# Performance work log

Hardware: AMD Instinct MI355X
Metric: run time of the kernel (lower is better)

The kernel has to match this reference:

```python
import jax, jax.numpy as jnp
import numpy as np

N = 100000
E = 1600000
F_IN = 256   # 4 * 64 after concat
H = 128

def _glorot(key, shape):
    fan_in, fan_out = shape
    lim = jnp.sqrt(6.0 / (fan_in + fan_out))
    return jax.random.uniform(key, shape, jnp.float32, -lim, lim)

def setup_inputs() -> dict:
    key = jax.random.key(0)
    ks = jax.random.split(key, 32)
    inp = {
        'x': jax.random.normal(ks[0], (N, 64), jnp.float32),
        'diff': jax.random.normal(ks[1], (N, 64), jnp.float32),
        'rec_prev': jax.random.normal(ks[2], (N, 64), jnp.float32),
        'hidden_prev': jax.random.normal(ks[3], (N, 64), jnp.float32),
        'edge_index': jax.random.randint(ks[4], (2, E), 0, N, jnp.int64),
    }
    dims = [(F_IN, H), (H, H), (H, H), (H, 1)]
    for i, (din, dout) in enumerate(dims):
        inp[f'Wl{i}'] = _glorot(ks[5 + 3 * i], (din, dout))  # neighbor (aggr) weight
        inp[f'Wr{i}'] = _glorot(ks[6 + 3 * i], (din, dout))  # root weight
        inp[f'b{i}'] = jnp.zeros((dout,), jnp.float32)
    return inp

def _sage_conv(h, src, dst, Wl, Wr, b):
    # mean aggregation of source-node features at destination nodes (PyG SAGEConv)
    msg_sum = jax.ops.segment_sum(h[src], dst, num_segments=N)        # [N, F]
    cnt = jax.ops.segment_sum(jnp.ones((src.shape[0],), h.dtype), dst, num_segments=N)
    mean = msg_sum / jnp.maximum(cnt, 1.0)[:, None]
    return mean @ Wl + h @ Wr + b

def reference(x, diff, rec_prev, hidden_prev, edge_index,
              Wl0, Wr0, b0, Wl1, Wr1, b1, Wl2, Wr2, b2, Wl3, Wr3, b3):
    src, dst = edge_index[0], edge_index[1]
    h = jnp.concatenate([x, diff, rec_prev, hidden_prev], axis=1)  # [N, 256]
    params = [(Wl0, Wr0, b0), (Wl1, Wr1, b1), (Wl2, Wr2, b2), (Wl3, Wr3, b3)]
    h = _sage_conv(h, src, dst, *params[0])
    for Wl, Wr, b in params[1:]:
        h = jax.nn.relu(h)
        h = _sage_conv(h, src, dst, Wl, Wr, b)
    out = jax.nn.sigmoid(h)          # [N, 1]
    lwp_util = jnp.mean(out)
    return out, lwp_util
```

## Files before the change

kernel.cpp:

```cpp
#include <hip/hip_runtime.h>
#include <hip/hip_bf16.h>

#define NN 100000
#define EE 1600000
#define HH 128
#define NB 391
#define CAP 5120
#define GB 1563
#define SB 256
#define EPB (EE / SB)

typedef short bf16x8 __attribute__((ext_vector_type(8)));
typedef short bf16x4 __attribute__((ext_vector_type(4)));
typedef float f32x4  __attribute__((ext_vector_type(4)));

__device__ inline short f2bf(float v) {
    __hip_bfloat16 b = __float2bfloat16(v);
    return *reinterpret_cast<short*>(&b);
}

typedef __attribute__((address_space(1))) void gvoid_t;
typedef __attribute__((address_space(3))) void svoid_t;
__device__ __forceinline__ void gload16(const void* g, void* l) {
    __builtin_amdgcn_global_load_lds((gvoid_t*)g, (svoid_t*)l, 16, 0, 0);
}

__device__ __forceinline__ void ld_fence() { asm volatile("" ::: "memory"); }

template <int N>
__device__ __forceinline__ void wait_vm_bar() {
    if constexpr (N == 0)
        asm volatile("s_waitcnt vmcnt(0)\n\ts_barrier" ::: "memory");
    else if constexpr (N == 2)
        asm volatile("s_waitcnt vmcnt(2)\n\ts_barrier" ::: "memory");
    else if constexpr (N == 4)
        asm volatile("s_waitcnt vmcnt(4)\n\ts_barrier" ::: "memory");
    else if constexpr (N == 8)
        asm volatile("s_waitcnt vmcnt(8)\n\ts_barrier" ::: "memory");
    else if constexpr (N == 12)
        asm volatile("s_waitcnt vmcnt(12)\n\ts_barrier" ::: "memory");
    else
        static_assert(N == 0 || N == 2 || N == 4 || N == 8 || N == 12, "bad N");
}
__device__ __forceinline__ void barrier_only() {
    asm volatile("s_barrier" ::: "memory");
}

__global__ __launch_bounds__(1024) void prep_kernel(
    const float* __restrict__ Wl0, const float* __restrict__ Wr0,
    const float* __restrict__ Wl1, const float* __restrict__ Wr1,
    const float* __restrict__ Wl2, const float* __restrict__ Wr2,
    __hip_bfloat16* __restrict__ WT0, __hip_bfloat16* __restrict__ WT1,
    __hip_bfloat16* __restrict__ WT2, int* __restrict__ bcur) {
    const int t = threadIdx.x;
    if (blockIdx.x == 128) {
        if (t < NB) bcur[t] = 0;
        return;
    }
    int id = blockIdx.x * 1024 + t;
    if (id < 65536) {
        int k = id & 255, n = id >> 8;
        float v = (n < 128) ? Wl0[(size_t)k * 128 + n]
                            : Wr0[(size_t)k * 128 + (n - 128)];
        WT0[(size_t)n * 256 + k] = __float2bfloat16(v);
    } else {
        id -= 65536;
        int layer = id >> 15;
        int u = id & 32767;
        int k = u & 127, n = u >> 7;
        const float* Wl = layer ? Wl2 : Wl1;
        const float* Wr = layer ? Wr2 : Wr1;
        __hip_bfloat16* WT = layer ? WT2 : WT1;
        float v = (n < 128) ? Wl[(size_t)k * 128 + n]
                            : Wr[(size_t)k * 128 + (n - 128)];
        WT[(size_t)n * 128 + k] = __float2bfloat16(v);
    }
}

#define EW 264
template <int K, bool FIRST>
__device__ __forceinline__ void gemm_body(
    short* __restrict__ lsh, int bid,
    const __hip_bfloat16* hin,
    const float* __restrict__ x0, const float* __restrict__ x1,
    const float* __restrict__ x2, const float* __restrict__ x3,
    const __hip_bfloat16* __restrict__ wt, const float* __restrict__ bias,
    __hip_bfloat16* zout, __hip_bfloat16* __restrict__ rout) {
    const int t    = threadIdx.x;
    const int w    = t >> 6;
    const int lane = t & 63;
    const int quad = lane >> 4;
    const int l16  = lane & 15;
    const int n0   = bid * 64;

    constexpr int NS   = K / 64;
    constexpr int BUFB = FIRST ? 16384 : 8192;
    char* const lc = (char*)lsh;

    const __hip_bfloat16* afeat[4];
#pragma unroll
    for (int ft = 0; ft < 4; ++ft)
        afeat[ft] = wt + (size_t)(w * 64 + ft * 16 + l16) * K + quad * 8;

    f32x4 acc[4][4];
#pragma unroll
    for (int ft = 0; ft < 4; ++ft)
#pragma unroll
        for (int nt = 0; nt < 4; ++nt)
            acc[ft][nt] = (f32x4){0.f, 0.f, 0.f, 0.f};

    bf16x8 wreg[NS][8];

    auto loadW = [&](int p) {
#pragma unroll
        for (int kcl = 0; kcl < 2; ++kcl)
#pragma unroll
            for (int ft = 0; ft < 4; ++ft)
                wreg[p][kcl * 4 + ft] =
                    *(const bf16x8*)(afeat[ft] + (p * 2 + kcl) * 32);
    };

    auto stage = [&](int p) {
        char* lb = lc + p * BUFB;
        if constexpr (FIRST) {
            const float* sp = (p == 0) ? x0 : (p == 1) ? x1 : (p == 2) ? x2 : x3;
#pragma unroll
            for (int i = 0; i < 4; ++i) {
                const int j   = w * 4 + i;
                const int row = j * 4 + (lane >> 4);
                int rg = n0 + row; if (rg > NN - 1) rg = NN - 1;
                const int colb = ((lane & 15) * 16) ^ ((row & 15) << 4);
                gload16((const char*)sp + (size_t)rg * 256 + colb, lb + j * 1024);
            }
        } else {
#pragma unroll
            for (int i = 0; i < 2; ++i) {
                const int j   = w * 2 + i;
                const int row = j * 8 + (lane >> 3);
                int rg = n0 + row; if (rg > NN - 1) rg = NN - 1;
                const int colb = ((lane & 7) * 16) ^ ((row & 7) << 4);
                gload16((const char*)hin + (size_t)rg * 256 + p * 128 + colb,
                        lb + j * 1024);
            }
        }
    };

    auto compute = [&](int s) {
        const char* lb = lc + s * BUFB;
#pragma unroll
        for (int kcl = 0; kcl < 2; ++kcl) {
#pragma unroll
            for (int nt = 0; nt < 4; ++nt) {
                const int row = nt * 16 + l16;
                bf16x8 b;
                if constexpr (FIRST) {
                    const int sw = (row & 15) << 4;
                    const int B0 = kcl * 128 + quad * 32;
                    const char* rb = lb + row * 256;
                    const f32x4 lo = *(const f32x4*)(rb + ((B0) ^ sw));
                    const f32x4 hi = *(const f32x4*)(rb + ((B0 + 16) ^ sw));
                    b[0] = f2bf(lo[0]); b[1] = f2bf(lo[1]);
                    b[2] = f2bf(lo[2]); b[3] = f2bf(lo[3]);
                    b[4] = f2bf(hi[0]); b[5] = f2bf(hi[1]);
                    b[6] = f2bf(hi[2]); b[7] = f2bf(hi[3]);
                } else {
                    const int sw = (row & 7) << 4;
                    const int B0 = kcl * 64 + quad * 16;
                    b = *(const bf16x8*)(lb + row * 128 + (B0 ^ sw));
                }
#pragma unroll
                for (int ft = 0; ft < 4; ++ft)
                    acc[ft][nt] = __builtin_amdgcn_mfma_f32_16x16x32_bf16(
                        wreg[s][kcl * 4 + ft], b, acc[ft][nt], 0, 0, 0);
            }
        }
    };

    if constexpr (FIRST) {
        loadW(0); loadW(1); loadW(2); loadW(3); ld_fence();
        stage(0); ld_fence();
        stage(1); ld_fence();
        stage(2); ld_fence();
        stage(3); ld_fence();
        wait_vm_bar<12>(); compute(0);
        wait_vm_bar<8>();  compute(1);
        wait_vm_bar<4>();  compute(2);
        wait_vm_bar<0>();  compute(3);
        barrier_only();
    } else {
        loadW(0); loadW(1); ld_fence();
        stage(0); ld_fence();
        stage(1); ld_fence();
        wait_vm_bar<2>(); compute(0);
        wait_vm_bar<0>(); compute(1);
        barrier_only();
    }

#pragma unroll
    for (int ft = 0; ft < 4; ++ft) {
        const int fb = ft * 16 + quad * 4;
        float4 bv = make_float4(0.f, 0.f, 0.f, 0.f);
        if (w >= 2) bv = *(const float4*)&bias[(w - 2) * 64 + fb];
        const int cbase = (w & 1) * 64 + ((w >= 2) ? 128 : 0);
#pragma unroll
        for (int nt = 0; nt < 4; ++nt) {
            const f32x4 a = acc[ft][nt];
            bf16x4 p;
            p[0] = f2bf(a[0] + bv.x); p[1] = f2bf(a[1] + bv.y);
            p[2] = f2bf(a[2] + bv.z); p[3] = f2bf(a[3] + bv.w);
            *(bf16x4*)&lsh[(nt * 16 + l16) * EW + cbase + fb] = p;
        }
    }
    __syncthreads();
#pragma unroll
    for (int u = 0; u < 8; ++u) {
        const int id  = u * 256 + t;
        const int row = id >> 5, ch = (id & 31) * 8;
        const int nd  = n0 + row;
        if (nd < NN) {
            const bf16x8 v = *(const bf16x8*)&lsh[row * EW + ch];
            if (ch < 128) *(bf16x8*)&zout[(size_t)nd * HH + ch] = v;
            else          *(bf16x8*)&rout[(size_t)nd * HH + (ch - 128)] = v;
        }
    }
}

__global__ __launch_bounds__(256, 2) void gemm0_kernel(
    const float* __restrict__ x0, const float* __restrict__ x1,
    const float* __restrict__ x2, const float* __restrict__ x3,
    const __hip_bfloat16* __restrict__ wt, const float* __restrict__ bias,
    __hip_bfloat16* __restrict__ zout, __hip_bfloat16* __restrict__ rout) {
    __shared__ short lsh[32768];
    gemm_body<256, true>(lsh, blockIdx.x, nullptr, x0, x1, x2, x3,
                         wt, bias, zout, rout);
}

template <int K>
__global__ __launch_bounds__(256) void gemm_kernel(
    const __hip_bfloat16* hin,
    const __hip_bfloat16* __restrict__ wt, const float* __restrict__ bias,
    __hip_bfloat16* zout, __hip_bfloat16* __restrict__ rout) {
    __shared__ short lsh[16896];
    gemm_body<K, false>(lsh, blockIdx.x, hin, nullptr, nullptr, nullptr, nullptr,
                        wt, bias, zout, rout);
}

__global__ __launch_bounds__(256) void scatter_kernel(
    const int* __restrict__ srcv, const int* __restrict__ dstv,
    int* __restrict__ bcur, int* __restrict__ pairs) {
    __shared__ int hist[NB];
    __shared__ int base[NB];
    const int t = threadIdx.x;

    for (int j = t; j < NB; j += 256) hist[j] = 0;
    __syncthreads();

    const int e0    = blockIdx.x * EPB;
    const int eend_ = e0 + EPB;

    for (int be = e0; be < eend_; be += 4096) {
        int d[16];
#pragma unroll
        for (int u = 0; u < 16; ++u) {
            const int e = be + u * 256 + t;
            d[u] = (e < eend_) ? dstv[e] : -1;
        }
#pragma unroll
        for (int u = 0; u < 16; ++u)
            if (d[u] >= 0) atomicAdd(&hist[d[u] >> 8], 1);
    }
    __syncthreads();

    for (int j = t; j < NB; j += 256)
        base[j] = hist[j] ? atomicAdd(&bcur[j], hist[j]) : 0;
    __syncthreads();
    for (int j = t; j < NB; j += 256) hist[j] = base[j];
    __syncthreads();

    for (int be = e0; be < eend_; be += 4096) {
        int s[16], d[16];
#pragma unroll
        for (int u = 0; u < 16; ++u) {
            const int e = be + u * 256 + t;
            if (e < eend_) { s[u] = srcv[e]; d[u] = dstv[e]; }
            else d[u] = -1;
        }
#pragma unroll
        for (int u = 0; u < 16; ++u)
            if (d[u] >= 0) {
                const int b   = d[u] >> 8;
                const int pos = atomicAdd(&hist[b], 1);
                if (pos < CAP) pairs[b * CAP + pos] = (s[u] << 8) | (d[u] & 255);
            }
    }
}

__global__ __launch_bounds__(256) void finalize_kernel(
    const int* __restrict__ bcur, const int* __restrict__ pairs,
    int* __restrict__ csr, int* __restrict__ beg, int* __restrict__ eend,
    float* __restrict__ inv) {
    __shared__ int cnt[256];
    __shared__ int scn[256];
    __shared__ int cur[256];
    const int b = blockIdx.x, t = threadIdx.x;
    int m = bcur[b];
    if (m > CAP) m = CAP;

    cnt[t] = 0;
    __syncthreads();
    for (int e = t; e < m; e += 256)
        atomicAdd(&cnt[pairs[b * CAP + e] & 255], 1);
    __syncthreads();

    const int v = cnt[t];
    scn[t] = v;
    __syncthreads();
    for (int st = 1; st < 256; st <<= 1) {
        int tv = (t >= st) ? scn[t - st] : 0;
        __syncthreads();
        scn[t] += tv;
        __syncthreads();
    }
    const int myStart = scn[t] - v;
    cur[t] = myStart;
    __syncthreads();

    for (int e = t; e < m; e += 256) {
        const int pk  = pairs[b * CAP + e];
        const int pos = atomicAdd(&cur[pk & 255], 1);
        csr[b * CAP + pos] = pk >> 8;
    }

    const int node = b * 256 + t;
    if (node < NN) {
        beg[node]  = b * CAP + myStart;
        eend[node] = b * CAP + myStart + v;
        inv[node]  = 1.0f / fmaxf((float)v, 1.0f);
    }
}

template <bool LAST>
__global__ __launch_bounds__(256) void aggregate_kernel(
    const __hip_bfloat16* __restrict__ z, __hip_bfloat16* __restrict__ rio,
    const int* __restrict__ beg, const int* __restrict__ eend,
    const int* __restrict__ csr, const float* __restrict__ inv,
    const float* __restrict__ Wl3, const float* __restrict__ Wr3,
    const float* __restrict__ b3, float* __restrict__ z3,
    float* __restrict__ r3) {
    const int i    = (blockIdx.x * 256 + threadIdx.x) >> 6;
    const int lane = threadIdx.x & 63;
    const int g    = lane >> 4;
    const int l16  = lane & 15;
    if (i >= NN) return;
    const int b0 = beg[i], e0 = eend[i];

    float acc[8];
#pragma unroll
    for (int j = 0; j < 8; ++j) acc[j] = 0.f;

    int e = b0 + g;
    for (; e + 12 < e0; e += 16) {
        const int s0 = csr[e];
        const int s1 = csr[e + 4];
        const int s2 = csr[e + 8];
        const int s3 = csr[e + 12];
        const bf16x8 z0 = *(const bf16x8*)&z[(size_t)s0 * HH + l16 * 8];
        const bf16x8 z1 = *(const bf16x8*)&z[(size_t)s1 * HH + l16 * 8];
        const bf16x8 z2 = *(const bf16x8*)&z[(size_t)s2 * HH + l16 * 8];
        const bf16x8 z3v = *(const bf16x8*)&z[(size_t)s3 * HH + l16 * 8];
        const __hip_bfloat162* p0 = (const __hip_bfloat162*)&z0;
        const __hip_bfloat162* p1 = (const __hip_bfloat162*)&z1;
        const __hip_bfloat162* p2 = (const __hip_bfloat162*)&z2;
        const __hip_bfloat162* p3 = (const __hip_bfloat162*)&z3v;
#pragma unroll
        for (int j = 0; j < 4; ++j) {
            acc[2 * j]     += __bfloat162float(p0[j].x) + __bfloat162float(p1[j].x)
                            + __bfloat162float(p2[j].x) + __bfloat162float(p3[j].x);
            acc[2 * j + 1] += __bfloat162float(p0[j].y) + __bfloat162float(p1[j].y)
                            + __bfloat162float(p2[j].y) + __bfloat162float(p3[j].y);
        }
    }
    for (; e < e0; e += 4) {
        const int s0 = csr[e];
        const bf16x8 z0 = *(const bf16x8*)&z[(size_t)s0 * HH + l16 * 8];
        const __hip_bfloat162* p0 = (const __hip_bfloat162*)&z0;
#pragma unroll
        for (int j = 0; j < 4; ++j) {
            acc[2 * j]     += __bfloat162float(p0[j].x);
            acc[2 * j + 1] += __bfloat162float(p0[j].y);
        }
    }

#pragma unroll
    for (int j = 0; j < 8; ++j) {
        acc[j] += __shfl_xor(acc[j], 16, 64);
        acc[j] += __shfl_xor(acc[j], 32, 64);
    }

    const float iv = inv[i];
    const int   f  = l16 * 8 + g * 2;
    const __hip_bfloat162 rv = *(const __hip_bfloat162*)&rio[(size_t)i * HH + f];
    const float ox = fmaxf(acc[g * 2]     * iv + __bfloat162float(rv.x), 0.f);
    const float oy = fmaxf(acc[g * 2 + 1] * iv + __bfloat162float(rv.y), 0.f);

    if (!LAST) {
        __hip_bfloat162 o;
        o.x = __float2bfloat16(ox);
        o.y = __float2bfloat16(oy);
        *(__hip_bfloat162*)&rio[(size_t)i * HH + f] = o;
    } else {
        const float2 wl = *(const float2*)&Wl3[f];
        const float2 wr = *(const float2*)&Wr3[f];
        float al = ox * wl.x + oy * wl.y;
        float ar = ox * wr.x + oy * wr.y;
#pragma unroll
        for (int m = 32; m; m >>= 1) {
            al += __shfl_xor(al, m, 64);
            ar += __shfl_xor(ar, m, 64);
        }
        if (lane == 0) {
            z3[i] = al;
            r3[i] = ar + b3[0];
        }
    }
}

__global__ __launch_bounds__(256) void final_kernel(
    const float* __restrict__ z3, const float* __restrict__ r3,
    const int* __restrict__ beg, const int* __restrict__ eend,
    const int* __restrict__ csr, const float* __restrict__ inv,
    float* __restrict__ out, float* __restrict__ partial) {
    __shared__ float red[4];
    const int i    = (blockIdx.x * 256 + threadIdx.x) >> 6;
    const int lane = threadIdx.x & 63;
    const int w    = threadIdx.x >> 6;
    float v = 0.f;
    if (i < NN) {
        const int b0 = beg[i], e0 = eend[i];
        float a = 0.f;
        for (int e = b0 + lane; e < e0; e += 64) a += z3[csr[e]];
#pragma unroll
        for (int m = 32; m; m >>= 1) a += __shfl_xor(a, m, 64);
        const float pre = a * inv[i] + r3[i];
        const float s = 1.f / (1.f + __expf(-pre));
        if (lane == 0) { out[i] = s; v = s; }
    }
    if (lane == 0) red[w] = v;
    __syncthreads();
    if (threadIdx.x == 0)
        partial[blockIdx.x] = red[0] + red[1] + red[2] + red[3];
}

__global__ __launch_bounds__(256) void mean_kernel(const float* __restrict__ partial,
                                                   int nb, float* __restrict__ out) {
    __shared__ float lds[256];
    float s = 0.f;
    for (int i = threadIdx.x; i < nb; i += 256) s += partial[i];
    lds[threadIdx.x] = s;
    __syncthreads();
    for (int st = 128; st; st >>= 1) {
        if (threadIdx.x < st) lds[threadIdx.x] += lds[threadIdx.x + st];
        __syncthreads();
    }
    if (threadIdx.x == 0) out[NN] = lds[0] / (float)NN;
}

extern "C" void kernel_launch(void* const* d_in, const int* in_sizes, int n_in,
                              void* d_out, int out_size, void* d_ws, size_t ws_size,
                              hipStream_t stream) {
    const float* x    = (const float*)d_in[0];
    const float* diff = (const float*)d_in[1];
    const float* rec  = (const float*)d_in[2];
    const float* hid  = (const float*)d_in[3];
    const int* edge   = (const int*)d_in[4];
    const int* esrc = edge;
    const int* edst = edge + EE;
    const float* Wl0 = (const float*)d_in[5];
    const float* Wr0 = (const float*)d_in[6];
    const float* b0  = (const float*)d_in[7];
    const float* Wl1 = (const float*)d_in[8];
    const float* Wr1 = (const float*)d_in[9];
    const float* b1  = (const float*)d_in[10];
    const float* Wl2 = (const float*)d_in[11];
    const float* Wr2 = (const float*)d_in[12];
    const float* b2  = (const float*)d_in[13];
    const float* Wl3 = (const float*)d_in[14];
    const float* Wr3 = (const float*)d_in[15];
    const float* b3  = (const float*)d_in[16];
    float* out = (float*)d_out;

    char* w = (char*)d_ws;
    auto alloc = [&](size_t bytes) -> void* {
        void* p = (void*)w;
        w += (bytes + 255) & ~(size_t)255;
        return p;
    };
    __hip_bfloat16* bufA = (__hip_bfloat16*)alloc((size_t)NN * HH * 2);
    __hip_bfloat16* bufB = (__hip_bfloat16*)alloc((size_t)NN * HH * 2);
    __hip_bfloat16* WT0  = (__hip_bfloat16*)alloc((size_t)256 * 256 * 2);
    __hip_bfloat16* WT1  = (__hip_bfloat16*)alloc((size_t)256 * 128 * 2);
    __hip_bfloat16* WT2  = (__hip_bfloat16*)alloc((size_t)256 * 128 * 2);
    int*   pairs   = (int*)alloc((size_t)NB * CAP * 4);
    int*   csr     = (int*)alloc((size_t)NB * CAP * 4);
    int*   bcur    = (int*)alloc((size_t)512 * 4);
    int*   beg     = (int*)alloc((size_t)NN * 4);
    int*   eend    = (int*)alloc((size_t)NN * 4);
    float* inv     = (float*)alloc((size_t)NN * 4);
    float* z3      = (float*)alloc((size_t)NN * 4);
    float* r3      = (float*)alloc((size_t)NN * 4);
    float* partial = (float*)alloc((size_t)25000 * 4);

    const int WB = (NN + 3) / 4;

    prep_kernel<<<129, 1024, 0, stream>>>(Wl0, Wr0, Wl1, Wr1, Wl2, Wr2,
                                          WT0, WT1, WT2, bcur);

    scatter_kernel<<<SB, 256, 0, stream>>>(esrc, edst, bcur, pairs);

    gemm0_kernel<<<GB, 256, 0, stream>>>(x, diff, rec, hid, WT0, b0, bufA, bufB);

    finalize_kernel<<<NB, 256, 0, stream>>>(bcur, pairs, csr, beg, eend, inv);

    aggregate_kernel<false><<<WB, 256, 0, stream>>>(bufA, bufB, beg, eend, csr, inv,
                                                    nullptr, nullptr, nullptr,
                                                    nullptr, nullptr);

    gemm_kernel<128><<<GB, 256, 0, stream>>>(bufB, WT1, b1, bufB, bufA);
    aggregate_kernel<false><<<WB, 256, 0, stream>>>(bufB, bufA, beg, eend, csr, inv,
                                                    nullptr, nullptr, nullptr,
                                                    nullptr, nullptr);

    gemm_kernel<128><<<GB, 256, 0, stream>>>(bufA, WT2, b2, bufA, bufB);
    aggregate_kernel<true><<<WB, 256, 0, stream>>>(bufA, bufB, beg, eend, csr, inv,
                                                   Wl3, Wr3, b3, z3, r3);

    final_kernel<<<WB, 256, 0, stream>>>(z3, r3, beg, eend, csr, inv, out, partial);
    mean_kernel<<<1, 256, 0, stream>>>(partial, WB, out);
}
```

Before: 512.4 us.

## Make GEMM kernels semi-persistent with cross-tile double-buffered pipelining

```diff
diff --git a/kernel.cpp b/kernel.cpp
--- a/kernel.cpp
+++ b/kernel.cpp
@@ -7,6 +7,8 @@
 #define NB 391
 #define CAP 5120
 #define GB 1563
+#define PT 3
+#define PBK 521
 #define SB 256
 #define EPB (EE / SB)
 
@@ -37,10 +39,13 @@
         asm volatile("s_waitcnt vmcnt(4)\n\ts_barrier" ::: "memory");
     else if constexpr (N == 8)
         asm volatile("s_waitcnt vmcnt(8)\n\ts_barrier" ::: "memory");
+    else if constexpr (N == 10)
+        asm volatile("s_waitcnt vmcnt(10)\n\ts_barrier" ::: "memory");
     else if constexpr (N == 12)
         asm volatile("s_waitcnt vmcnt(12)\n\ts_barrier" ::: "memory");
     else
-        static_assert(N == 0 || N == 2 || N == 4 || N == 8 || N == 12, "bad N");
+        static_assert(N == 0 || N == 2 || N == 4 || N == 8 || N == 10 || N == 12,
+                      "bad N");
 }
 __device__ __forceinline__ void barrier_only() {
     asm volatile("s_barrier" ::: "memory");
@@ -79,8 +84,8 @@
 
 #define EW 264
 template <int K, bool FIRST>
-__device__ __forceinline__ void gemm_body(
-    short* __restrict__ lsh, int bid,
+__device__ __forceinline__ void gemm_persist(
+    short* __restrict__ lsh,
     const __hip_bfloat16* hin,
     const float* __restrict__ x0, const float* __restrict__ x1,
     const float* __restrict__ x2, const float* __restrict__ x3,
@@ -91,11 +96,12 @@
     const int lane = t & 63;
     const int quad = lane >> 4;
     const int l16  = lane & 15;
-    const int n0   = bid * 64;
-
-    constexpr int NS   = K / 64;
+    const int g0   = blockIdx.x * PT;
+
+    constexpr int SPT  = K / 64;
     constexpr int BUFB = FIRST ? 16384 : 8192;
-    char* const lc = (char*)lsh;
+    char*  const lc  = (char*)lsh;
+    short* const eph = (short*)(lc + 2 * BUFB);
 
     const __hip_bfloat16* afeat[4];
 #pragma unroll
@@ -109,19 +115,12 @@
         for (int nt = 0; nt < 4; ++nt)
             acc[ft][nt] = (f32x4){0.f, 0.f, 0.f, 0.f};
 
-    bf16x8 wreg[NS][8];
-
-    auto loadW = [&](int p) {
-#pragma unroll
-        for (int kcl = 0; kcl < 2; ++kcl)
-#pragma unroll
-            for (int ft = 0; ft < 4; ++ft)
-                wreg[p][kcl * 4 + ft] =
-                    *(const bf16x8*)(afeat[ft] + (p * 2 + kcl) * 32);
-    };
-
-    auto stage = [&](int p) {
-        char* lb = lc + p * BUFB;
+    bf16x8 wreg[SPT][8];
+
+    auto stage = [&](int q) {
+        const int n0 = (g0 + q / SPT) * 64;
+        const int p  = q % SPT;
+        char* lb = lc + (q & 1) * BUFB;
         if constexpr (FIRST) {
             const float* sp = (p == 0) ? x0 : (p == 1) ? x1 : (p == 2) ? x2 : x3;
 #pragma unroll
@@ -145,8 +144,9 @@
         }
     };
 
-    auto compute = [&](int s) {
-        const char* lb = lc + s * BUFB;
+    auto compute = [&](int q) {
+        const char* lb = lc + (q & 1) * BUFB;
+        const int   s  = q % SPT;
 #pragma unroll
         for (int kcl = 0; kcl < 2; ++kcl) {
 #pragma unroll
@@ -176,52 +176,73 @@
         }
     };
 
+    auto epi = [&](int tl) {
+        const int n0 = (g0 + tl) * 64;
+#pragma unroll
+        for (int ft = 0; ft < 4; ++ft) {
+            const int fb = ft * 16 + quad * 4;
+            float4 bv = make_float4(0.f, 0.f, 0.f, 0.f);
+            if (w >= 2) bv = *(const float4*)&bias[(w - 2) * 64 + fb];
+            const int cbase = (w & 1) * 64 + ((w >= 2) ? 128 : 0);
+#pragma unroll
+            for (int nt = 0; nt < 4; ++nt) {
+                const f32x4 a = acc[ft][nt];
+                bf16x4 p;
+                p[0] = f2bf(a[0] + bv.x); p[1] = f2bf(a[1] + bv.y);
+                p[2] = f2bf(a[2] + bv.z); p[3] = f2bf(a[3] + bv.w);
+                *(bf16x4*)&eph[(nt * 16 + l16) * EW + cbase + fb] = p;
+                acc[ft][nt] = (f32x4){0.f, 0.f, 0.f, 0.f};
+            }
+        }
+        asm volatile("s_waitcnt lgkmcnt(0)\n\ts_barrier" ::: "memory");
+#pragma unroll
+        for (int u = 0; u < 8; ++u) {
+            const int id  = u * 256 + t;
+            const int row = id >> 5, ch = (id & 31) * 8;
+            const int nd  = n0 + row;
+            if (nd < NN) {
+                const bf16x8 v = *(const bf16x8*)&eph[row * EW + ch];
+                if (ch < 128) *(bf16x8*)&zout[(size_t)nd * HH + ch] = v;
+                else          *(bf16x8*)&rout[(size_t)nd * HH + (ch - 128)] = v;
+            }
+        }
+        ld_fence();
+    };
+
+#pragma unroll
+    for (int p = 0; p < SPT; ++p)
+#pragma unroll
+        for (int kcl = 0; kcl < 2; ++kcl)
+#pragma unroll
+            for (int ft = 0; ft < 4; ++ft)
+                wreg[p][kcl * 4 + ft] =
+                    *(const bf16x8*)(afeat[ft] + (p * 2 + kcl) * 32);
+    ld_fence();
+    stage(0); ld_fence();
+    stage(1); ld_fence();
+
     if constexpr (FIRST) {
-        loadW(0); loadW(1); loadW(2); loadW(3); ld_fence();
-        stage(0); ld_fence();
-        stage(1); ld_fence();
-        stage(2); ld_fence();
-        stage(3); ld_fence();
-        wait_vm_bar<12>(); compute(0);
-        wait_vm_bar<8>();  compute(1);
-        wait_vm_bar<4>();  compute(2);
-        wait_vm_bar<0>();  compute(3);
-        barrier_only();
+        wait_vm_bar<4>();  compute(0);  barrier_only(); stage(2);  ld_fence();
+        wait_vm_bar<4>();  compute(1);  barrier_only(); stage(3);  ld_fence();
+        wait_vm_bar<4>();  compute(2);  barrier_only(); stage(4);  ld_fence();
+        wait_vm_bar<4>();  compute(3);  barrier_only(); stage(5);  ld_fence(); epi(0);
+        wait_vm_bar<12>(); compute(4);  barrier_only(); stage(6);  ld_fence();
+        wait_vm_bar<12>(); compute(5);  barrier_only(); stage(7);  ld_fence();
+        wait_vm_bar<4>();  compute(6);  barrier_only(); stage(8);  ld_fence();
+        wait_vm_bar<4>();  compute(7);  barrier_only(); stage(9);  ld_fence(); epi(1);
+        wait_vm_bar<12>(); compute(8);  barrier_only(); stage(10); ld_fence();
+        wait_vm_bar<12>(); compute(9);  barrier_only(); stage(11); ld_fence();
+        wait_vm_bar<4>();  compute(10); barrier_only();
+        wait_vm_bar<0>();  compute(11);
+        epi(2);
     } else {
-        loadW(0); loadW(1); ld_fence();
-        stage(0); ld_fence();
-        stage(1); ld_fence();
-        wait_vm_bar<2>(); compute(0);
-        wait_vm_bar<0>(); compute(1);
-        barrier_only();
-    }
-
-#pragma unroll
-    for (int ft = 0; ft < 4; ++ft) {
-        const int fb = ft * 16 + quad * 4;
-        float4 bv = make_float4(0.f, 0.f, 0.f, 0.f);
-        if (w >= 2) bv = *(const float4*)&bias[(w - 2) * 64 + fb];
-        const int cbase = (w & 1) * 64 + ((w >= 2) ? 128 : 0);
-#pragma unroll
-        for (int nt = 0; nt < 4; ++nt) {
-            const f32x4 a = acc[ft][nt];
-            bf16x4 p;
-            p[0] = f2bf(a[0] + bv.x); p[1] = f2bf(a[1] + bv.y);
-            p[2] = f2bf(a[2] + bv.z); p[3] = f2bf(a[3] + bv.w);
-            *(bf16x4*)&lsh[(nt * 16 + l16) * EW + cbase + fb] = p;
-        }
-    }
-    __syncthreads();
-#pragma unroll
-    for (int u = 0; u < 8; ++u) {
-        const int id  = u * 256 + t;
-        const int row = id >> 5, ch = (id & 31) * 8;
-        const int nd  = n0 + row;
-        if (nd < NN) {
-            const bf16x8 v = *(const bf16x8*)&lsh[row * EW + ch];
-            if (ch < 128) *(bf16x8*)&zout[(size_t)nd * HH + ch] = v;
-            else          *(bf16x8*)&rout[(size_t)nd * HH + (ch - 128)] = v;
-        }
+        wait_vm_bar<2>();  compute(0); barrier_only(); stage(2); ld_fence();
+        wait_vm_bar<2>();  compute(1); barrier_only(); stage(3); ld_fence(); epi(0);
+        wait_vm_bar<10>(); compute(2); barrier_only(); stage(4); ld_fence();
+        wait_vm_bar<10>(); compute(3); barrier_only(); stage(5); ld_fence(); epi(1);
+        wait_vm_bar<10>(); compute(4); barrier_only();
+        wait_vm_bar<8>();  compute(5);
+        epi(2);
     }
 }
 
@@ -230,19 +251,18 @@
     const float* __restrict__ x2, const float* __restrict__ x3,
     const __hip_bfloat16* __restrict__ wt, const float* __restrict__ bias,
     __hip_bfloat16* __restrict__ zout, __hip_bfloat16* __restrict__ rout) {
-    __shared__ short lsh[32768];
-    gemm_body<256, true>(lsh, blockIdx.x, nullptr, x0, x1, x2, x3,
-                         wt, bias, zout, rout);
+    __shared__ short lsh[33280];
+    gemm_persist<256, true>(lsh, nullptr, x0, x1, x2, x3, wt, bias, zout, rout);
 }
 
 template <int K>
-__global__ __launch_bounds__(256) void gemm_kernel(
+__global__ __launch_bounds__(256, 2) void gemm_kernel(
     const __hip_bfloat16* hin,
     const __hip_bfloat16* __restrict__ wt, const float* __restrict__ bias,
     __hip_bfloat16* zout, __hip_bfloat16* __restrict__ rout) {
-    __shared__ short lsh[16896];
-    gemm_body<K, false>(lsh, blockIdx.x, hin, nullptr, nullptr, nullptr, nullptr,
-                        wt, bias, zout, rout);
+    __shared__ short lsh[25088];
+    gemm_persist<K, false>(lsh, hin, nullptr, nullptr, nullptr, nullptr,
+                           wt, bias, zout, rout);
 }
 
 __global__ __launch_bounds__(256) void scatter_kernel(
@@ -517,7 +537,7 @@
 
     scatter_kernel<<<SB, 256, 0, stream>>>(esrc, edst, bcur, pairs);
 
-    gemm0_kernel<<<GB, 256, 0, stream>>>(x, diff, rec, hid, WT0, b0, bufA, bufB);
+    gemm0_kernel<<<PBK, 256, 0, stream>>>(x, diff, rec, hid, WT0, b0, bufA, bufB);
 
     finalize_kernel<<<NB, 256, 0, stream>>>(bcur, pairs, csr, beg, eend, inv);
 
@@ -525,12 +545,12 @@
                                                     nullptr, nullptr, nullptr,
                                                     nullptr, nullptr);
 
-    gemm_kernel<128><<<GB, 256, 0, stream>>>(bufB, WT1, b1, bufB, bufA);
+    gemm_kernel<128><<<PBK, 256, 0, stream>>>(bufB, WT1, b1, bufB, bufA);
     aggregate_kernel<false><<<WB, 256, 0, stream>>>(bufB, bufA, beg, eend, csr, inv,
                                                     nullptr, nullptr, nullptr,
                                                     nullptr, nullptr);
 
-    gemm_kernel<128><<<GB, 256, 0, stream>>>(bufA, WT2, b2, bufA, bufB);
+    gemm_kernel<128><<<PBK, 256, 0, stream>>>(bufA, WT2, b2, bufA, bufB);
     aggregate_kernel<true><<<WB, 256, 0, stream>>>(bufA, bufB, beg, eend, csr, inv,
                                                    Wl3, Wr3, b3, z3, r3);
 
```

Result: slower. 528.7 us (+3.2%).
